# Kernel tuning notes

Measured on AMD Instinct MI355X. Metric: run time of the kernel, lower is better.

## Reference

```python
import math
import jax, jax.numpy as jnp
import numpy as np

NUM_HEADS = 16


def setup_inputs() -> dict:
    key = jax.random.key(0)
    ks = jax.random.split(key, 5)
    B, S, H = 2, 2048, 1024
    hidden_states = jax.random.normal(ks[0], (B, S, H), dtype=jnp.float32)
    # causal lower-triangular float mask [1, 1, S, S], as the module expects
    ltor_mask = jnp.tril(jnp.ones((S, S), dtype=jnp.float32))[None, None, :, :]
    # weights stored pre-transposed: y = x @ W + b (equivalent to torch Linear)
    W_qkv = jax.random.normal(ks[1], (H, 3 * H), dtype=jnp.float32) * (1.0 / math.sqrt(H))
    b_qkv = jnp.zeros((3 * H,), dtype=jnp.float32)
    W_dense = jax.random.normal(ks[2], (H, H), dtype=jnp.float32) * (1.0 / math.sqrt(H))
    b_dense = jnp.zeros((H,), dtype=jnp.float32)
    return {
        "hidden_states": hidden_states,
        "ltor_mask": ltor_mask,
        "W_qkv": W_qkv,
        "b_qkv": b_qkv,
        "W_dense": W_dense,
        "b_dense": b_dense,
    }


def reference(hidden_states, ltor_mask, W_qkv, b_qkv, W_dense, b_dense):
    B, S, H = hidden_states.shape
    nh = NUM_HEADS
    hd = H // nh

    # fused QKV projection: [B, S, 3H] -> split -> [B, nh, S, hd]
    qkv = hidden_states @ W_qkv + b_qkv
    q, k, v = jnp.split(qkv, 3, axis=-1)

    def to_heads(x):
        return x.reshape(B, S, nh, hd).transpose(0, 2, 1, 3)

    q, k, v = to_heads(q), to_heads(k), to_heads(v)

    # scaled dot-product scores [B, nh, S, S]
    scores = jnp.einsum("bhqd,bhkd->bhqk", q, k) / math.sqrt(hd)
    # mul/sub causal masking, exactly as the torch module does
    scores = scores * ltor_mask - 10000.0 * (1.0 - ltor_mask)
    probs = jax.nn.softmax(scores, axis=-1)
    # attention dropout omitted (eval mode / p=0.0)

    ctx = jnp.einsum("bhqk,bhkd->bhqd", probs, v)
    ctx = ctx.transpose(0, 2, 1, 3).reshape(B, S, H)

    out = ctx @ W_dense + b_dense
    # output dropout omitted (eval mode / p=0.0)
    return out
```

## Files before the change

kernel.cpp:

```cpp
#include <hip/hip_runtime.h>
#include <math.h>

#define BATCH 2
#define SEQ   2048
#define HID   1024
#define NHEAD 16
#define HDIM  64
#define MTOT  (BATCH * SEQ)
#define QKVN  (3 * HID)
#define HBUF  ((size_t)BATCH * NHEAD * SEQ * HDIM)

typedef _Float16 f16x8 __attribute__((ext_vector_type(8)));
typedef _Float16 f16x4 __attribute__((ext_vector_type(4)));
typedef float    f32x4 __attribute__((ext_vector_type(4)));

#define MFMA16(a, b, c) __builtin_amdgcn_mfma_f32_16x16x32_f16((a), (b), (c), 0, 0, 0)

#define GLDS16(gp, lp) __builtin_amdgcn_global_load_lds( \
    (const __attribute__((address_space(1))) void*)(gp), \
    (__attribute__((address_space(3))) void*)(lp), 16, 0, 0)

#if __has_builtin(__builtin_amdgcn_exp2f)
#define EXP2F(x) __builtin_amdgcn_exp2f(x)
#else
#define EXP2F(x) exp2f(x)
#endif

#define SCALE2 0.18033688011f
#define MASK2  -14426.950408f
#define BIAS2  -4.0f

#define SWZ4(row) (((row) & 3) ^ (((row) >> 2) & 3))

__global__ __launch_bounds__(256) void prep_kernel(
    const float* __restrict__ hs, const float* __restrict__ Wqkv,
    const float* __restrict__ Wd, _Float16* __restrict__ A_h,
    _Float16* __restrict__ outQ, _Float16* __restrict__ outD)
{
    __shared__ _Float16 T[32][36];
    const int gid = blockIdx.x;
    const int tid = threadIdx.x;
    if (gid < 2048) {
        const int ci = gid * 256 + tid;
        const int m = ci >> 7, cc = ci & 127;
        const int g = cc >> 2, c = cc & 3;
        const float* src = hs + (size_t)m * 1024 + cc * 8;
        f16x8 o;
#pragma unroll
        for (int j = 0; j < 8; ++j) o[j] = (_Float16)src[j];
        *(f16x8*)(A_h + (size_t)m * 1024 + g * 32 + ((c ^ SWZ4(m)) << 3)) = o;
        return;
    }
    const int tb = gid - 2048;
    const int bx = tb & 127, k0 = (tb >> 7) * 32;
    const float* in;
    _Float16* out;
    int N, n0;
    if (bx < 96) { in = Wqkv; out = outQ; N = QKVN; n0 = bx * 32; }
    else         { in = Wd;   out = outD; N = HID;  n0 = (bx - 96) * 32; }
    {
        const int r = tid >> 3, c4 = (tid & 7) * 4;
        float4 v = *(const float4*)(in + (size_t)(k0 + r) * N + n0 + c4);
        T[r][c4 + 0] = (_Float16)v.x;
        T[r][c4 + 1] = (_Float16)v.y;
        T[r][c4 + 2] = (_Float16)v.z;
        T[r][c4 + 3] = (_Float16)v.w;
    }
    __syncthreads();
    {
        const int nn = tid >> 3, k4 = (tid & 7) * 4;
        const int n = n0 + nn;
        f16x4 o;
        o[0] = T[k4 + 0][nn]; o[1] = T[k4 + 1][nn];
        o[2] = T[k4 + 2][nn]; o[3] = T[k4 + 3][nn];
        const int pos = ((k4 >> 3) ^ SWZ4(n)), half = (k4 >> 2) & 1;
        *(f16x4*)(out + (size_t)n * 1024 + k0 + pos * 8 + half * 4) = o;
    }
}

template<int EPI, int TM>
__global__ __launch_bounds__(256) void mfma_gemm(
    const _Float16* __restrict__ A, const _Float16* __restrict__ Bt,
    const float* __restrict__ bias, void* __restrict__ Cout,
    int M, int N, int K)
{
    constexpr int SMEM_BYTES = (EPI == 0) ? 18432 : 17408;
    __shared__ __align__(16) char SMEM[SMEM_BYTES];
    _Float16* As = (_Float16*)SMEM;
    _Float16* Bs = As + TM * 32;
    constexpr int TI = TM / 32;
    constexpr int AR = TM / 4;

    const int tid = threadIdx.x;
    const int w = tid >> 6, l = tid & 63;
    const int a = l & 15, q4 = l >> 4;
    const int m0 = blockIdx.y * TM, n0 = blockIdx.x * 128;
    const int wm = (w >> 1) * (TM / 2), wn = (w & 1) * 64;

    f32x4 acc[TI][4];
#pragma unroll
    for (int i = 0; i < TI; ++i)
#pragma unroll
        for (int j = 0; j < 4; ++j) acc[i][j] = (f32x4){0.f, 0.f, 0.f, 0.f};

    const _Float16* gA = A + (size_t)(m0 + w * AR + (l >> 2)) * K + (l & 3) * 8;
    const _Float16* gB = Bt + (size_t)(n0 + w * 32 + (l >> 2)) * K + (l & 3) * 8;
    _Float16* sA = As + w * AR * 32;
    _Float16* sB = Bs + w * 1024;

    for (int k0 = 0; k0 < K; k0 += 32) {
#pragma unroll
        for (int u = 0; u < TM / 64; ++u)
            GLDS16(gA + (size_t)u * 16 * K + k0, sA + u * 512);
        GLDS16(gB + k0,          sB);
        GLDS16(gB + 16 * K + k0, sB + 512);
        __syncthreads();

        f16x8 af[TI], bf[4];
        const int pa = (q4 ^ SWZ4(a)) << 3;
#pragma unroll
        for (int i = 0; i < TI; ++i)
            af[i] = *(const f16x8*)&As[(wm + 16 * i + a) * 32 + pa];
#pragma unroll
        for (int j = 0; j < 4; ++j)
            bf[j] = *(const f16x8*)&Bs[(wn + 16 * j + a) * 32 + pa];
#pragma unroll
        for (int i = 0; i < TI; ++i)
#pragma unroll
            for (int j = 0; j < 4; ++j)
                acc[i][j] = MFMA16(af[i], bf[j], acc[i][j]);
        __syncthreads();
    }

    if (EPI == 0) {
        const int nbase = n0 + wn;
        const int t = nbase >> 10, h = (nbase >> 6) & 15;
        const int bb = (m0 + wm) >> 11;
        const int sbase = (m0 + wm) & 2047;
        _Float16* base = (_Float16*)Cout;
        _Float16* Cw = (_Float16*)SMEM + w * 2304;
        const int lsub = l >> 3, c = l & 7;
        if (t != 2) {
            const int cswz = (t == 1) ? (c ^ lsub) : c;
            _Float16* gq = base + (size_t)t * HBUF
                         + ((size_t)(bb * 16 + h) * 2048 + sbase) * 64;
#pragma unroll
            for (int pass = 0; pass < 2; ++pass) {
#pragma unroll
                for (int j = 0; j < 4; ++j) {
                    const float bv = bias[nbase + 16 * j + a];
#pragma unroll
                    for (int i2 = 0; i2 < 2; ++i2)
#pragma unroll
                        for (int r = 0; r < 4; ++r)
                            Cw[(16 * i2 + q4 * 4 + r) * 72 + 16 * j + a] =
                                (_Float16)(acc[2 * pass + i2][j][r] + bv);
                }
#pragma unroll
                for (int pp = 0; pp < 4; ++pp) {
                    const int lr = pp * 8 + lsub;
                    f16x8 v8 = *(const f16x8*)&Cw[lr * 72 + cswz * 8];
                    *(f16x8*)(gq + (size_t)(32 * pass + lr) * 64 + c * 8) = v8;
                }
            }
        } else {
            const int cswz = c ^ lsub;
            _Float16* gv = base + 2 * HBUF
                         + ((size_t)(bb * 16 + h) * 64) * 2048 + sbase;
#pragma unroll
            for (int pass = 0; pass < 2; ++pass) {
#pragma unroll
                for (int jj = 0; jj < 2; ++jj) {
                    const int j = 2 * pass + jj;
                    const float bv = bias[nbase + 16 * j + a];
#pragma unroll
                    for (int i = 0; i < 4; ++i) {
                        f16x4 pk;
#pragma unroll
                        for (int r = 0; r < 4; ++r)
                            pk[r] = (_Float16)(acc[i][j][r] + bv);
                        *(f16x4*)&Cw[(16 * jj + a) * 72 + 16 * i + q4 * 4] = pk;
                    }
                }
#pragma unroll
                for (int pp = 0; pp < 4; ++pp) {
                    const int dl = pp * 8 + lsub;
                    f16x8 v8 = *(const f16x8*)&Cw[dl * 72 + cswz * 8];
                    *(f16x8*)(gv + (size_t)(32 * pass + dl) * 2048 + c * 8) = v8;
                }
            }
        }
    } else {
        float* C = (float*)Cout;
        float* Cw = (float*)SMEM + w * 1088;
        const int lr = l >> 2, lc = l & 3;
#pragma unroll
        for (int i = 0; i < TI; ++i) {
#pragma unroll
            for (int j = 0; j < 4; ++j) {
                const float bv = bias[n0 + wn + 16 * j + a];
#pragma unroll
                for (int r = 0; r < 4; ++r)
                    Cw[(q4 * 4 + r) * 68 + 16 * j + a] = acc[i][j][r] + bv;
            }
            float* gout = C + (size_t)(m0 + wm + 16 * i + lr) * N + n0 + wn;
#pragma unroll
            for (int pp = 0; pp < 4; ++pp) {
                float4 v4 = *(const float4*)&Cw[lr * 68 + (lc + 4 * pp) * 4];
                *(float4*)(gout + (lc + 4 * pp) * 4) = v4;
            }
        }
    }
}

__global__ __launch_bounds__(256, 2) void attn_mfma(
    const _Float16* __restrict__ qb, const _Float16* __restrict__ kb,
    const _Float16* __restrict__ vtb, _Float16* __restrict__ ctx)
{
    __shared__ _Float16 Ks[2][64 * 64];
    __shared__ _Float16 VT[2][64 * 64];
    __shared__ _Float16 Ps[4][16 * 64];

    const int bid = blockIdx.x;
    const int jj = bid >> 3;
    const int bhIdx = (bid & 7) * 4 + (jj >> 4);
    const int p = jj & 15;
    const int b = bhIdx >> 4, h = bhIdx & 15;
    const int tid = threadIdx.x;
    const int w = tid >> 6, l = tid & 63;
    const int a = l & 15, q4 = l >> 4, a7 = a & 7;
    const size_t bh  = ((size_t)b * NHEAD + h) * SEQ;
    const size_t bhd = ((size_t)b * NHEAD + h) * 64;

    const int qHi = (31 - p) * 64 + w * 16;
    const int qLo = p * 64 + w * 16;
    const int ntiles = 32 - p;

    f16x8 qfh[2], qfl[2];
    {
        const _Float16* qp = qb + (bh + qHi + a) * 64;
        qfh[0] = *(const f16x8*)(qp + q4 * 8);
        qfh[1] = *(const f16x8*)(qp + 32 + q4 * 8);
        const _Float16* ql = qb + (bh + qLo + a) * 64;
        qfl[0] = *(const f16x8*)(ql + q4 * 8);
        qfl[1] = *(const f16x8*)(ql + 32 + q4 * 8);
    }

    f32x4 Oh[4], Ol[4];
#pragma unroll
    for (int c = 0; c < 4; ++c) {
        Oh[c] = (f32x4){0.f, 0.f, 0.f, 0.f};
        Ol[c] = (f32x4){0.f, 0.f, 0.f, 0.f};
    }
    float lh = 0.f, ll = 0.f;

    const _Float16* kg = kb + (bh + w * 16) * 64 + l * 8;
    const int vrow = w * 16 + (l >> 3);
    const _Float16* vg = vtb + (bhd + vrow) * 2048 + (l & 7) * 8;
    _Float16* pbuf = &Ps[w][0];
    const int p0 = (q4 ^ a7) << 3;

    auto stage = [&](int t, int buf) {
        _Float16* ksl = &Ks[buf][0] + w * 1024 + l * 8;
        const _Float16* kt = kg + (size_t)t * 4096;
        GLDS16(kt,       ksl);
        GLDS16(kt + 512, ksl + 512);
        _Float16* vtl = &VT[buf][0] + vrow * 64 + (l & 7) * 8;
        GLDS16(vg + t * 64,            vtl);
        GLDS16(vg + t * 64 + 8 * 2048, vtl + 512);
    };

    stage(0, 0);

    for (int t = 0; t < ntiles; ++t) {
        __syncthreads();
        if (t + 1 < ntiles) stage(t + 1, (t + 1) & 1);

        const _Float16* ksb  = &Ks[t & 1][0];
        const _Float16* vbuf = &VT[t & 1][0];
        const int kt0 = t * 64;
        const bool doLo = (t <= p);

        f32x4 sh[4], sl[4];
#pragma unroll
        for (int n0 = 0; n0 < 4; ++n0) {
            f16x8 kf0 = *(const f16x8*)&ksb[(n0 * 16 + a) * 64 + p0];
            f16x8 kf1 = *(const f16x8*)&ksb[(n0 * 16 + a) * 64 + (p0 ^ 32)];
            f32x4 c = (f32x4){0.f, 0.f, 0.f, 0.f};
            c = MFMA16(kf0, qfh[0], c);
            c = MFMA16(kf1, qfh[1], c);
            sh[n0] = c;
            if (doLo) {
                f32x4 d = (f32x4){0.f, 0.f, 0.f, 0.f};
                d = MFMA16(kf0, qfl[0], d);
                d = MFMA16(kf1, qfl[1], d);
                sl[n0] = d;
            }
        }

        auto softmax_P = [&](f32x4 st[4], float& lrun, const bool maskT,
                             const int qbase, f16x8& pf0, f16x8& pf1) {
            if (maskT) {
#pragma unroll
                for (int n0 = 0; n0 < 4; ++n0)
#pragma unroll
                    for (int r = 0; r < 4; ++r) {
                        const int kgl = kt0 + n0 * 16 + q4 * 4 + r;
                        st[n0][r] = (kgl > qbase + a) ? MASK2
                                                      : fmaf(st[n0][r], SCALE2, BIAS2);
                    }
            } else {
#pragma unroll
                for (int n0 = 0; n0 < 4; ++n0)
#pragma unroll
                    for (int r = 0; r < 4; ++r)
                        st[n0][r] = fmaf(st[n0][r], SCALE2, BIAS2);
            }
            float ls = 0.f;
#pragma unroll
            for (int n0 = 0; n0 < 4; ++n0)
#pragma unroll
                for (int r = 0; r < 4; ++r) {
                    const float pe = EXP2F(st[n0][r]);
                    st[n0][r] = pe;
                    ls += pe;
                }
            lrun += ls;
#pragma unroll
            for (int n0 = 0; n0 < 4; ++n0) {
                f16x4 pk;
#pragma unroll
                for (int r = 0; r < 4; ++r) pk[r] = (_Float16)st[n0][r];
                const int pos = (2 * n0 + (q4 >> 1)) ^ a7;
                *(f16x4*)&pbuf[a * 64 + pos * 8 + ((q4 & 1) << 2)] = pk;
            }
            pf0 = *(const f16x8*)&pbuf[a * 64 + p0];
            pf1 = *(const f16x8*)&pbuf[a * 64 + (p0 ^ 32)];
        };

        f16x8 pfh0, pfh1, pfl0, pfl1;
        softmax_P(sh, lh, t == 31 - p, qHi, pfh0, pfh1);
        if (doLo) softmax_P(sl, ll, t == p, qLo, pfl0, pfl1);

#pragma unroll
        for (int c = 0; c < 4; ++c) {
            f16x8 vf0 = *(const f16x8*)&vbuf[(c * 16 + a) * 64 + p0];
            f16x8 vf1 = *(const f16x8*)&vbuf[(c * 16 + a) * 64 + (p0 ^ 32)];
            Oh[c] = MFMA16(vf0, pfh0, Oh[c]);
            Oh[c] = MFMA16(vf1, pfh1, Oh[c]);
            if (doLo) {
                Ol[c] = MFMA16(vf0, pfl0, Ol[c]);
                Ol[c] = MFMA16(vf1, pfl1, Ol[c]);
            }
        }
    }

    auto finish = [&](float lrun, const f32x4* O, const int qbase) {
        float lt = lrun;
        lt += __shfl_xor(lt, 16);
        lt += __shfl_xor(lt, 32);
        const float inv = 1.0f / lt;
        const size_t row = (size_t)b * SEQ + qbase + a;
#pragma unroll
        for (int c = 0; c < 4; ++c) {
            const int d0 = c * 16 + q4 * 4;
            const int kcol = h * 64 + (d0 & ~31)
                           + ((((d0 >> 3) & 3) ^ SWZ4(a)) << 3) + (d0 & 7);
            f16x4 ov;
#pragma unroll
            for (int r = 0; r < 4; ++r) ov[r] = (_Float16)(O[c][r] * inv);
            *(f16x4*)(ctx + row * HID + kcol) = ov;
        }
    };
    finish(lh, Oh, qHi);
    finish(ll, Ol, qLo);
}

extern "C" void kernel_launch(void* const* d_in, const int* in_sizes, int n_in,
                              void* d_out, int out_size, void* d_ws, size_t ws_size,
                              hipStream_t stream) {
    const float* hs   = (const float*)d_in[0];
    const float* Wqkv = (const float*)d_in[2];
    const float* bqkv = (const float*)d_in[3];
    const float* Wd   = (const float*)d_in[4];
    const float* bd   = (const float*)d_in[5];

    _Float16* A_h   = (_Float16*)d_ws;
    _Float16* WqkvT = A_h + (size_t)MTOT * HID;
    _Float16* WdT   = WqkvT + (size_t)QKVN * HID;
    _Float16* qbuf  = WdT + (size_t)HID * HID;
    _Float16* ctxb  = qbuf + 3 * HBUF;

    prep_kernel<<<6144, 256, 0, stream>>>(hs, Wqkv, Wd, A_h, WqkvT, WdT);

    mfma_gemm<0, 128><<<dim3(QKVN / 128, MTOT / 128), 256, 0, stream>>>(
        A_h, WqkvT, bqkv, (void*)qbuf, MTOT, QKVN, HID);

    attn_mfma<<<512, 256, 0, stream>>>(
        qbuf, qbuf + HBUF, qbuf + 2 * HBUF, ctxb);

    mfma_gemm<1, 64><<<dim3(HID / 128, MTOT / 64), 256, 0, stream>>>(
        ctxb, WdT, bd, d_out, MTOT, HID, HID);
}
```

Before: 205.7 us.

## Pre-pack A operands in MFMA fragment order and load them directly to registers

The activation matrix (hidden states after conversion, and the attention context) is now written in a 16-row MFMA-fragment-major layout, so each lane of the GEMM can load its A fragment straight from global memory into registers without going through LDS. The GEMM register-prefetches the next A fragment and double-buffers the B tile in LDS, which leaves one barrier per k-step instead of two. The prep kernel stages 16 rows through LDS to perform the repack, and the attention epilogue writes ctx directly in the packed layout. This trades LDS traffic and barriers for uncoalesced-per-row but contiguous-per-wave global loads, and hardcodes K=1024 and N=HID.

```diff
diff --git a/kernel.cpp b/kernel.cpp
--- a/kernel.cpp
+++ b/kernel.cpp
@@ -32,26 +32,41 @@
 
 #define SWZ4(row) (((row) & 3) ^ (((row) >> 2) & 3))
 
+
 __global__ __launch_bounds__(256) void prep_kernel(
     const float* __restrict__ hs, const float* __restrict__ Wqkv,
     const float* __restrict__ Wd, _Float16* __restrict__ A_h,
     _Float16* __restrict__ outQ, _Float16* __restrict__ outD)
 {
-    __shared__ _Float16 T[32][36];
+    __shared__ __align__(16) _Float16 LB[16 * 1040];
     const int gid = blockIdx.x;
     const int tid = threadIdx.x;
-    if (gid < 2048) {
-        const int ci = gid * 256 + tid;
-        const int m = ci >> 7, cc = ci & 127;
-        const int g = cc >> 2, c = cc & 3;
-        const float* src = hs + (size_t)m * 1024 + cc * 8;
-        f16x8 o;
-#pragma unroll
-        for (int j = 0; j < 8; ++j) o[j] = (_Float16)src[j];
-        *(f16x8*)(A_h + (size_t)m * 1024 + g * 32 + ((c ^ SWZ4(m)) << 3)) = o;
+    if (gid < 256) {
+        const int m16 = gid;
+#pragma unroll
+        for (int p = 0; p < 8; ++p) {
+            const int task = p * 256 + tid;
+            const int row = task >> 7, cc = task & 127;
+            const float* src = hs + ((size_t)m16 * 16 + row) * 1024 + cc * 8;
+            f16x8 o;
+#pragma unroll
+            for (int j = 0; j < 8; ++j) o[j] = (_Float16)src[j];
+            *(f16x8*)&LB[row * 1040 + cc * 8] = o;
+        }
+        __syncthreads();
+        _Float16* dst = A_h + (size_t)m16 * 16384;
+#pragma unroll
+        for (int p = 0; p < 8; ++p) {
+            const int ci = p * 256 + tid;
+            const int k32 = ci >> 6, lane = ci & 63;
+            const int aa = lane & 15, qq = lane >> 4;
+            f16x8 v = *(const f16x8*)&LB[aa * 1040 + (k32 * 4 + qq) * 8];
+            *(f16x8*)(dst + (size_t)ci * 8) = v;
+        }
         return;
     }
-    const int tb = gid - 2048;
+    _Float16 (*T)[36] = (_Float16(*)[36])LB;
+    const int tb = gid - 256;
     const int bx = tb & 127, k0 = (tb >> 7) * 32;
     const float* in;
     _Float16* out;
@@ -81,15 +96,13 @@
 template<int EPI, int TM>
 __global__ __launch_bounds__(256) void mfma_gemm(
     const _Float16* __restrict__ A, const _Float16* __restrict__ Bt,
-    const float* __restrict__ bias, void* __restrict__ Cout,
-    int M, int N, int K)
+    const float* __restrict__ bias, void* __restrict__ Cout)
 {
     constexpr int SMEM_BYTES = (EPI == 0) ? 18432 : 17408;
     __shared__ __align__(16) char SMEM[SMEM_BYTES];
-    _Float16* As = (_Float16*)SMEM;
-    _Float16* Bs = As + TM * 32;
+    _Float16* Bs = (_Float16*)SMEM;
     constexpr int TI = TM / 32;
-    constexpr int AR = TM / 4;
+    constexpr int NI = 32;
 
     const int tid = threadIdx.x;
     const int w = tid >> 6, l = tid & 63;
@@ -103,34 +116,44 @@
 #pragma unroll
         for (int j = 0; j < 4; ++j) acc[i][j] = (f32x4){0.f, 0.f, 0.f, 0.f};
 
-    const _Float16* gA = A + (size_t)(m0 + w * AR + (l >> 2)) * K + (l & 3) * 8;
-    const _Float16* gB = Bt + (size_t)(n0 + w * 32 + (l >> 2)) * K + (l & 3) * 8;
-    _Float16* sA = As + w * AR * 32;
-    _Float16* sB = Bs + w * 1024;
-
-    for (int k0 = 0; k0 < K; k0 += 32) {
-#pragma unroll
-        for (int u = 0; u < TM / 64; ++u)
-            GLDS16(gA + (size_t)u * 16 * K + k0, sA + u * 512);
-        GLDS16(gB + k0,          sB);
-        GLDS16(gB + 16 * K + k0, sB + 512);
+    const _Float16* gB = Bt + (size_t)(n0 + w * 32 + (l >> 2)) * 1024 + (l & 3) * 8;
+    const _Float16* gA = A + ((size_t)((m0 + wm) >> 4) * 32) * 512 + l * 8;
+
+    auto stageB = [&](int t) {
+        _Float16* sB = Bs + ((t & 1) << 12) + w * 1024;
+        GLDS16(gB + t * 32,          sB);
+        GLDS16(gB + 16 * 1024 + t * 32, sB + 512);
+    };
+
+    f16x8 afc[TI], afn[TI];
+    stageB(0);
+#pragma unroll
+    for (int i = 0; i < TI; ++i)
+        afc[i] = *(const f16x8*)(gA + (size_t)i * 16384);
+
+    for (int t = 0; t < NI; ++t) {
         __syncthreads();
-
-        f16x8 af[TI], bf[4];
+        if (t + 1 < NI) {
+#pragma unroll
+            for (int i = 0; i < TI; ++i)
+                afn[i] = *(const f16x8*)(gA + (size_t)i * 16384 + (t + 1) * 512);
+            stageB(t + 1);
+        }
+        const _Float16* bs = Bs + ((t & 1) << 12);
+        f16x8 bf[4];
         const int pa = (q4 ^ SWZ4(a)) << 3;
 #pragma unroll
+        for (int j = 0; j < 4; ++j)
+            bf[j] = *(const f16x8*)&bs[(wn + 16 * j + a) * 32 + pa];
+#pragma unroll
         for (int i = 0; i < TI; ++i)
-            af[i] = *(const f16x8*)&As[(wm + 16 * i + a) * 32 + pa];
-#pragma unroll
-        for (int j = 0; j < 4; ++j)
-            bf[j] = *(const f16x8*)&Bs[(wn + 16 * j + a) * 32 + pa];
-#pragma unroll
-        for (int i = 0; i < TI; ++i)
 #pragma unroll
             for (int j = 0; j < 4; ++j)
-                acc[i][j] = MFMA16(af[i], bf[j], acc[i][j]);
-        __syncthreads();
-    }
+                acc[i][j] = MFMA16(afc[i], bf[j], acc[i][j]);
+#pragma unroll
+        for (int i = 0; i < TI; ++i) afc[i] = afn[i];
+    }
+    __syncthreads();
 
     if (EPI == 0) {
         const int nbase = n0 + wn;
@@ -203,7 +226,7 @@
                 for (int r = 0; r < 4; ++r)
                     Cw[(q4 * 4 + r) * 68 + 16 * j + a] = acc[i][j][r] + bv;
             }
-            float* gout = C + (size_t)(m0 + wm + 16 * i + lr) * N + n0 + wn;
+            float* gout = C + (size_t)(m0 + wm + 16 * i + lr) * HID + n0 + wn;
 #pragma unroll
             for (int pp = 0; pp < 4; ++pp) {
                 float4 v4 = *(const float4*)&Cw[lr * 68 + (lc + 4 * pp) * 4];
@@ -360,16 +383,17 @@
         lt += __shfl_xor(lt, 16);
         lt += __shfl_xor(lt, 32);
         const float inv = 1.0f / lt;
-        const size_t row = (size_t)b * SEQ + qbase + a;
+        const int m16 = (b * SEQ + qbase) >> 4;
+        _Float16* dst = ctx + (size_t)m16 * 16384;
 #pragma unroll
         for (int c = 0; c < 4; ++c) {
-            const int d0 = c * 16 + q4 * 4;
-            const int kcol = h * 64 + (d0 & ~31)
-                           + ((((d0 >> 3) & 3) ^ SWZ4(a)) << 3) + (d0 & 7);
+            const int k32   = h * 2 + (c >> 1);
+            const int lanep = ((c & 1) * 2 + (q4 >> 1)) * 16 + a;
+            const int j0    = (q4 & 1) * 4;
             f16x4 ov;
 #pragma unroll
             for (int r = 0; r < 4; ++r) ov[r] = (_Float16)(O[c][r] * inv);
-            *(f16x4*)(ctx + row * HID + kcol) = ov;
+            *(f16x4*)(dst + ((size_t)k32 * 64 + lanep) * 8 + j0) = ov;
         }
     };
     finish(lh, Oh, qHi);
@@ -391,14 +415,14 @@
     _Float16* qbuf  = WdT + (size_t)HID * HID;
     _Float16* ctxb  = qbuf + 3 * HBUF;
 
-    prep_kernel<<<6144, 256, 0, stream>>>(hs, Wqkv, Wd, A_h, WqkvT, WdT);
+    prep_kernel<<<4352, 256, 0, stream>>>(hs, Wqkv, Wd, A_h, WqkvT, WdT);
 
     mfma_gemm<0, 128><<<dim3(QKVN / 128, MTOT / 128), 256, 0, stream>>>(
-        A_h, WqkvT, bqkv, (void*)qbuf, MTOT, QKVN, HID);
+        A_h, WqkvT, bqkv, (void*)qbuf);
 
     attn_mfma<<<512, 256, 0, stream>>>(
         qbuf, qbuf + HBUF, qbuf + 2 * HBUF, ctxb);
 
     mfma_gemm<1, 64><<<dim3(HID / 128, MTOT / 64), 256, 0, stream>>>(
-        ctxb, WdT, bd, d_out, MTOT, HID, HID);
+        ctxb, WdT, bd, d_out);
 }
```

Measured after the change: 197.7 us. -3.9%, faster.
